# Performance work log

Measured on AMD Instinct MI355X. Metric: run time of the kernel, lower is better.

The kernel has to match this reference:

```python
import jax, jax.numpy as jnp
import numpy as np

HIDDEN = 1024
FFN = 3584
N_EXPERTS = 8
TOP_K = 2


def setup_inputs() -> dict:
    key = jax.random.key(0)
    ks = jax.random.split(key, 5)
    B, S = 2, 2048
    hidden_states = jax.random.normal(ks[0], (B, S, HIDDEN), dtype=jnp.float32)
    # gate: Linear(hidden, n_experts, bias=False); stored as [H, E] so y = x @ gate_w
    gate_w = jax.random.normal(ks[1], (HIDDEN, N_EXPERTS), dtype=jnp.float32) * (HIDDEN ** -0.5)
    # stacked expert weights: w1 (gate proj), w3 (up proj): [E, H, F]; w2 (down proj): [E, F, H]
    w1 = jax.random.normal(ks[2], (N_EXPERTS, HIDDEN, FFN), dtype=jnp.float32) * (HIDDEN ** -0.5)
    w3 = jax.random.normal(ks[3], (N_EXPERTS, HIDDEN, FFN), dtype=jnp.float32) * (HIDDEN ** -0.5)
    w2 = jax.random.normal(ks[4], (N_EXPERTS, FFN, HIDDEN), dtype=jnp.float32) * (FFN ** -0.5)
    return {"hidden_states": hidden_states, "gate_w": gate_w, "w1": w1, "w2": w2, "w3": w3}


def reference(hidden_states, gate_w, w1, w2, w3):
    B, S, H = hidden_states.shape
    x = hidden_states.reshape(-1, H)  # [T, H]
    T = x.shape[0]
    router_logits = x @ gate_w  # [T, E]
    # softmax in fp32 as in original
    routing_weights = jax.nn.softmax(router_logits.astype(jnp.float32), axis=-1)
    top_w, selected = jax.lax.top_k(routing_weights, TOP_K)  # [T, k]
    top_w = top_w / jnp.sum(top_w, axis=-1, keepdims=True)
    top_w = top_w.astype(x.dtype)
    # scatter top-k weights into dense per-expert combine weights [T, E];
    # zero weight for unselected experts reproduces the sparse gather/scatter math exactly
    combine = jnp.zeros((T, N_EXPERTS), dtype=x.dtype).at[
        jnp.arange(T)[:, None], selected
    ].add(top_w)
    # expert gated MLP, all experts batched: [T, E, F]
    g = jnp.einsum('th,ehf->tef', x, w1)
    u = jnp.einsum('th,ehf->tef', x, w3)
    h = jax.nn.silu(g) * u
    # down-proj fused with weighted combine: avoids [T, E, H] intermediate
    final_hidden_states = jnp.einsum('tef,efh,te->th', h, w2, combine)
    return final_hidden_states, router_logits
```

## Files before the change

kernel.cpp:

```cpp
#include <hip/hip_runtime.h>
#include <hip/hip_bf16.h>
#include <cstdint>
#include <cstddef>

#define T_TOK 4096
#define HID   1024
#define FFN   3584
#define FFI   (2 * FFN)
#define NEXP  8
#define RTOT  (T_TOK * 2)
#define MAXT  72
#define BM 128
#define BN 128
#define BK 64
#define NT1 (FFI / BN)
#define NT2 (HID / BN)
#define SPLITK2 2
#define KCH2 (FFN / SPLITK2)
#define CPAD 32
#define G1BLKS (NT1 * MAXT)
#define W2TBLKS ((HID/64)*(FFN/64)*NEXP)
#define RTRBLKS (T_TOK / 4)
#define DTBLKS  ((FFN/64)*(HID/64)*2*NEXP)

typedef __attribute__((ext_vector_type(8))) short bvec8;
typedef __attribute__((ext_vector_type(4))) short bvec4;
typedef __attribute__((ext_vector_type(4))) float fvec4;
typedef unsigned short u16;

__device__ __forceinline__ u16 f2b(float f) {
  __bf16 b = (__bf16)f;
  return __builtin_bit_cast(u16, b);
}
__device__ __forceinline__ float b2f(u16 u) {
  unsigned v = (unsigned)u << 16;
  return __builtin_bit_cast(float, v);
}

__device__ __forceinline__ void gload16(const u16* g, u16* l) {
  __builtin_amdgcn_global_load_lds((const __attribute__((address_space(1))) void*)g,
                                   (__attribute__((address_space(3))) void*)l, 16, 0, 0);
}

__device__ __forceinline__ int xcd_swz(int bid, int nwg) {
  int q = nwg >> 3, r = nwg & 7;
  int xcd = bid & 7, sub = bid >> 3;
  return (xcd < r ? xcd * (q + 1) : r * (q + 1) + (xcd - r) * q) + sub;
}


__device__ void router_body(const float* __restrict__ x, const float* __restrict__ gw,
                            float* __restrict__ logits, int* __restrict__ tk_id,
                            float* __restrict__ tk_w, int* __restrict__ counts,
                            u16* __restrict__ xb, int blk, int tid) {
  const int lane = tid & 63;
  const int wid  = tid >> 6;
  const int t = blk * 4 + wid;
  const float4* xr = (const float4*)(x + (size_t)t * HID);
  float acc[NEXP] = {0.f, 0.f, 0.f, 0.f, 0.f, 0.f, 0.f, 0.f};
#pragma unroll
  for (int it = 0; it < 4; ++it) {
    int k4 = it * 64 + lane;
    float4 xv = xr[k4];
    if (xb) {
      bvec4 o;
      o[0] = (short)f2b(xv.x); o[1] = (short)f2b(xv.y);
      o[2] = (short)f2b(xv.z); o[3] = (short)f2b(xv.w);
      *(bvec4*)(xb + (size_t)t * HID + k4 * 4) = o;
    }
    const float* gp = gw + (size_t)k4 * 4 * NEXP;
    float xs[4] = {xv.x, xv.y, xv.z, xv.w};
#pragma unroll
    for (int kk = 0; kk < 4; ++kk) {
      float4 ga = ((const float4*)(gp + kk * NEXP))[0];
      float4 gb = ((const float4*)(gp + kk * NEXP))[1];
      acc[0] += xs[kk] * ga.x; acc[1] += xs[kk] * ga.y;
      acc[2] += xs[kk] * ga.z; acc[3] += xs[kk] * ga.w;
      acc[4] += xs[kk] * gb.x; acc[5] += xs[kk] * gb.y;
      acc[6] += xs[kk] * gb.z; acc[7] += xs[kk] * gb.w;
    }
  }
#pragma unroll
  for (int off = 32; off > 0; off >>= 1) {
#pragma unroll
    for (int e = 0; e < NEXP; ++e) acc[e] += __shfl_xor(acc[e], off, 64);
  }
  if (lane < NEXP) logits[(size_t)t * NEXP + lane] = acc[lane];
  if (tk_id && lane == 0) {
    int e0 = 0; float l0 = acc[0];
#pragma unroll
    for (int e = 1; e < NEXP; ++e) if (acc[e] > l0) { l0 = acc[e]; e0 = e; }
    int e1 = -1; float l1 = -3.4e38f;
#pragma unroll
    for (int e = 0; e < NEXP; ++e) if (e != e0 && acc[e] > l1) { l1 = acc[e]; e1 = e; }
    float w0 = 1.f / (1.f + expf(l1 - l0));
    float w1 = 1.f - w0;
    tk_id[t * 2 + 0] = e0; tk_id[t * 2 + 1] = e1;
    tk_w[t * 2 + 0] = w0;  tk_w[t * 2 + 1] = w1;
    atomicAdd(&counts[e0 * CPAD], 1); atomicAdd(&counts[e1 * CPAD], 1);
  }
}

__device__ void dualT_body(const float* __restrict__ w1, const float* __restrict__ w3,
                           u16* __restrict__ bi, int bx, int by, int bz, int t,
                           u16* __restrict__ tile) {
  const int e = bz >> 1, half = bz & 1;
  const float* src = (half ? w3 : w1) + (size_t)e * HID * FFN;
  u16* dst = bi + (size_t)e * FFI * HID;
  const int c0 = bx * 64, r0 = by * 64;
  const int m = t & 15;
  const int g = t >> 4;
  u16 v[4][4];
#pragma unroll
  for (int i = 0; i < 4; ++i) {
    float4 q = *(const float4*)(src + (size_t)(r0 + 4 * g + i) * FFN + c0 + 4 * m);
    v[i][0] = f2b(q.x); v[i][1] = f2b(q.y); v[i][2] = f2b(q.z); v[i][3] = f2b(q.w);
  }
  const int phys = (g ^ ((m & 3) << 2)) * 4;
#pragma unroll
  for (int j = 0; j < 4; ++j) {
    int c = 4 * m + j;
    bvec4 o; o[0] = (short)v[0][j]; o[1] = (short)v[1][j];
    o[2] = (short)v[2][j]; o[3] = (short)v[3][j];
    *(bvec4*)&tile[c * 72 + phys] = o;
  }
  __syncthreads();
  const int cl = t >> 2;
  const int q  = t & 3;
  const int base = ((q ^ ((cl >> 2) & 3)) << 4);
  bvec8 ra = *(const bvec8*)&tile[cl * 72 + base];
  bvec8 rb = *(const bvec8*)&tile[cl * 72 + base + 8];
  const int orow = (c0 << 1) + ((cl >> 4) << 5) + (cl & 15) + (half << 4);
  u16* dp = dst + (size_t)orow * HID + r0 + 16 * q;
  *(bvec8*)(dp + 0) = ra;
  *(bvec8*)(dp + 8) = rb;
}

__device__ void w2T_body(const float* __restrict__ w2, u16* __restrict__ w2t,
                         int bx, int by, int e, int t, u16* __restrict__ tile) {
  const float* src = w2 + (size_t)e * FFN * HID;
  u16* dst = w2t + (size_t)e * HID * FFN;
  const int c0 = bx * 64, r0 = by * 64;
  const int m = t & 15;
  const int g = t >> 4;
  u16 v[4][4];
#pragma unroll
  for (int i = 0; i < 4; ++i) {
    float4 q = *(const float4*)(src + (size_t)(r0 + 4 * g + i) * HID + c0 + 4 * m);
    v[i][0] = f2b(q.x); v[i][1] = f2b(q.y); v[i][2] = f2b(q.z); v[i][3] = f2b(q.w);
  }
  const int phys = (g ^ ((m & 3) << 2)) * 4;
#pragma unroll
  for (int j = 0; j < 4; ++j) {
    int c = 4 * m + j;
    bvec4 o; o[0] = (short)v[0][j]; o[1] = (short)v[1][j];
    o[2] = (short)v[2][j]; o[3] = (short)v[3][j];
    *(bvec4*)&tile[c * 72 + phys] = o;
  }
  __syncthreads();
  const int cl = t >> 2;
  const int q  = t & 3;
  const int base = ((q ^ ((cl >> 2) & 3)) << 4);
  bvec8 ra = *(const bvec8*)&tile[cl * 72 + base];
  bvec8 rb = *(const bvec8*)&tile[cl * 72 + base + 8];
  u16* dp = dst + (size_t)(c0 + cl) * FFN + r0 + 16 * q;
  *(bvec8*)(dp + 0) = ra;
  *(bvec8*)(dp + 8) = rb;
}

__device__ void gemm1_body(const u16* __restrict__ xb, const u16* __restrict__ bi,
                           const int* __restrict__ rowmap, const int4* __restrict__ tilemap,
                           u16* __restrict__ hbuf, int bid, int tid,
                           u16* __restrict__ As, u16* __restrict__ Bs) {
  const int wg = xcd_swz(bid, NT1 * MAXT);
  const int mt = wg % MAXT;
  const int nt = wg / MAXT;
  int4 ti = tilemap[mt];
  if (ti.x < 0) return;
  const int e = ti.x, rowbase = ti.y, mvalid = ti.z;
  const int n0 = nt * BN;

  const int lane = tid & 63;
  const int wv = tid >> 6;
  const int srow = tid >> 3;
  const int csrc = ((tid & 7) ^ (srow & 7)) * 8;
  const u16* wb = bi + (size_t)e * FFI * HID;
  const u16* gA[4]; const u16* gB[4];
  u16* lA[4]; u16* lB[4];
#pragma unroll
  for (int r = 0; r < 4; ++r) {
    int row = r * 32 + srow;
    int tok = rowmap[min(rowbase + row, RTOT - 1)];
    gA[r] = xb + (size_t)tok * HID + csrc;
    gB[r] = wb + (size_t)(n0 + row) * HID + csrc;
    lA[r] = &As[(r * 32 + wv * 8) * BK];
    lB[r] = &Bs[(r * 32 + wv * 8) * BK];
  }

  const int wm = (tid >> 7) & 1, wn = (tid >> 6) & 1;
  const int l15 = lane & 15;
  const int kg = lane >> 4;
  const int swz = l15 & 7;
  const int aBase = (wm * 64 + l15) * BK;
  const int bBase = (wn * 64 + l15) * BK;
  const int ch0 = ((0 + kg) ^ swz) * 8;
  const int ch1 = ((4 + kg) ^ swz) * 8;

  fvec4 acc[4][4] = {};

  for (int kt = 0; kt < HID / BK; ++kt) {
#pragma unroll
    for (int r = 0; r < 4; ++r) { gload16(gA[r], lA[r]); gA[r] += BK; }
#pragma unroll
    for (int r = 0; r < 4; ++r) { gload16(gB[r], lB[r]); gB[r] += BK; }
    __syncthreads();
    bvec8 a0[4], a1[4];
#pragma unroll
    for (int mi = 0; mi < 4; ++mi) {
      a0[mi] = *(const bvec8*)&As[aBase + mi * 16 * BK + ch0];
      a1[mi] = *(const bvec8*)&As[aBase + mi * 16 * BK + ch1];
    }
#pragma unroll
    for (int ni = 0; ni < 4; ++ni) {
      bvec8 b0 = *(const bvec8*)&Bs[bBase + ni * 16 * BK + ch0];
#pragma unroll
      for (int mi = 0; mi < 4; ++mi)
        acc[mi][ni] = __builtin_amdgcn_mfma_f32_16x16x32_bf16(a0[mi], b0, acc[mi][ni], 0, 0, 0);
      bvec8 b1 = *(const bvec8*)&Bs[bBase + ni * 16 * BK + ch1];
#pragma unroll
      for (int mi = 0; mi < 4; ++mi)
        acc[mi][ni] = __builtin_amdgcn_mfma_f32_16x16x32_bf16(a1[mi], b1, acc[mi][ni], 0, 0, 0);
    }
    __syncthreads();
  }
  const int rg4 = (lane >> 4) * 4;
#pragma unroll
  for (int mi = 0; mi < 4; ++mi) {
#pragma unroll
    for (int j = 0; j < 4; ++j) {
      int ml = wm * 64 + mi * 16 + rg4 + j;
      if (ml < mvalid) {
        size_t rowoff = (size_t)(rowbase + ml) * FFN + ((n0 + wn * 64) >> 1);
#pragma unroll
        for (int np = 0; np < 2; ++np) {
          float g = acc[mi][2 * np][j], u = acc[mi][2 * np + 1][j];
          float hv = (g / (1.f + expf(-g))) * u;
          hbuf[rowoff + np * 16 + l15] = f2b(hv);
        }
      }
    }
  }
}


__global__ void fused_pre_kernel(const float* __restrict__ x, const float* __restrict__ gw,
                                 const float* __restrict__ w1, const float* __restrict__ w3,
                                 float* __restrict__ logits, int* __restrict__ tk_id,
                                 float* __restrict__ tk_w, int* __restrict__ counts,
                                 u16* __restrict__ xb, u16* __restrict__ bi) {
  __shared__ __attribute__((aligned(16))) u16 tile[64 * 72];
  const int bid = blockIdx.x;
  if (bid < RTRBLKS) {
    router_body(x, gw, logits, tk_id, tk_w, counts, xb, bid, threadIdx.x);
  } else {
    int did = bid - RTRBLKS;
    int bx = did % (FFN / 64); int rest = did / (FFN / 64);
    int by = rest % (HID / 64); int bz = rest / (HID / 64);
    dualT_body(w1, w3, bi, bx, by, bz, threadIdx.x, tile);
  }
}

__launch_bounds__(256, 3)
__global__ void fused_g1w2_kernel(const u16* __restrict__ xb, const u16* __restrict__ bi,
                                  const int* __restrict__ rowmap,
                                  const int4* __restrict__ tilemap, u16* __restrict__ hbuf,
                                  const float* __restrict__ w2, u16* __restrict__ w2t) {
  __shared__ __attribute__((aligned(128))) u16 As[BM * BK];
  __shared__ __attribute__((aligned(128))) u16 Bs[BN * BK];
  const int bid = blockIdx.x;
  if (bid < G1BLKS) {
    gemm1_body(xb, bi, rowmap, tilemap, hbuf, bid, threadIdx.x, As, Bs);
  } else {
    int id = bid - G1BLKS;
    int bx = id % (HID / 64); int rest = id / (HID / 64);
    int by = rest % (FFN / 64); int e = rest / (FFN / 64);
    w2T_body(w2, w2t, bx, by, e, threadIdx.x, As);
  }
}

__global__ void router_kernel(const float* __restrict__ x, const float* __restrict__ gw,
                              float* __restrict__ logits, int* __restrict__ tk_id,
                              float* __restrict__ tk_w, int* __restrict__ counts,
                              u16* __restrict__ xb) {
  router_body(x, gw, logits, tk_id, tk_w, counts, xb, blockIdx.x, threadIdx.x);
}
__global__ void transpose_cast_dual_kernel(const float* __restrict__ w1,
                                           const float* __restrict__ w3,
                                           u16* __restrict__ bi) {
  __shared__ __attribute__((aligned(16))) u16 tile[64 * 72];
  dualT_body(w1, w3, bi, blockIdx.x, blockIdx.y, blockIdx.z, threadIdx.x, tile);
}
__global__ void transpose_cast_w2_kernel(const float* __restrict__ w2, u16* __restrict__ w2t) {
  __shared__ __attribute__((aligned(16))) u16 tile[64 * 72];
  w2T_body(w2, w2t, blockIdx.x, blockIdx.y, blockIdx.z, threadIdx.x, tile);
}
__launch_bounds__(256, 3)
__global__ void gemm1_kernel(const u16* __restrict__ xb, const u16* __restrict__ bi,
                             const int* __restrict__ rowmap,
                             const int4* __restrict__ tilemap, u16* __restrict__ hbuf) {
  __shared__ __attribute__((aligned(128))) u16 As[BM * BK];
  __shared__ __attribute__((aligned(128))) u16 Bs[BN * BK];
  gemm1_body(xb, bi, rowmap, tilemap, hbuf, blockIdx.x, threadIdx.x, As, Bs);
}

__global__ void scan_kernel(const int* __restrict__ counts, int* __restrict__ offsets,
                            int* __restrict__ cursors, int4* __restrict__ tilemap) {
  __shared__ int c[NEXP];
  __shared__ int tbase[NEXP + 1];
  const int t = threadIdx.x;
  if (t < NEXP) c[t] = counts[t * CPAD];
  __syncthreads();
  if (t < NEXP) {
    int off = 0, tiles = 0;
    for (int e = 0; e < t; ++e) { off += c[e]; tiles += (c[e] + BM - 1) / BM; }
    offsets[t] = off; cursors[t * CPAD] = 0;
    if (t == NEXP - 1) {
      offsets[NEXP] = off + c[t];
      tbase[NEXP] = tiles + (c[t] + BM - 1) / BM;
    }
    tbase[t] = tiles;
    const int cc = c[t];
    for (int tm = 0; tm * BM < cc; ++tm)
      tilemap[tiles + tm] = make_int4(t, off + tm * BM, min(BM, cc - tm * BM), 0);
  }
  __syncthreads();
  for (int i = tbase[NEXP] + t; i < MAXT; i += 64)
    tilemap[i] = make_int4(-1, 0, 0, 0);
}

__global__ void scatter_kernel(const int* __restrict__ tk_id, const float* __restrict__ tk_w,
                               const int* __restrict__ offsets, int* __restrict__ cursors,
                               int* __restrict__ rowmap, float* __restrict__ roww,
                               int* __restrict__ tokrow) {
  int i = blockIdx.x * 256 + threadIdx.x;
  int t = i >> 1;
  int e = tk_id[i]; float w = tk_w[i];
  const int lane = threadIdx.x & 63;
  const unsigned long long lt = (lane == 63) ? ~0ull >> 1 : (1ull << lane) - 1ull;
  int base = 0, rank = 0;
#pragma unroll
  for (int ex = 0; ex < NEXP; ++ex) {
    unsigned long long m = __ballot(e == ex);
    if (e == ex) {
      int cnt = __popcll(m);
      int leader = __ffsll((long long)m) - 1;
      int b = 0;
      if (lane == leader) b = atomicAdd(&cursors[ex * CPAD], cnt);
      b = __shfl(b, leader, 64);
      base = b; rank = __popcll(m & lt);
    }
  }
  int r = offsets[e] + base + rank;
  rowmap[r] = t; roww[r] = w;
  tokrow[i] = r;
}

__launch_bounds__(256, 3)
__global__ void gemm2_kernel(const u16* __restrict__ hbuf, const u16* __restrict__ w2t,
                             const float* __restrict__ roww,
                             const int4* __restrict__ tilemap, u16* __restrict__ part) {
  const int wg = xcd_swz(blockIdx.x, NT2 * MAXT * SPLITK2);
  const int mt = wg % MAXT;
  const int rest = wg / MAXT;
  const int nt = rest % NT2;
  const int sk = rest / NT2;
  int4 ti = tilemap[mt];
  if (ti.x < 0) return;
  const int e = ti.x, rowbase = ti.y, mvalid = ti.z;
  const int n0 = nt * BN;
  const int k0 = sk * KCH2;

  __shared__ __attribute__((aligned(128))) u16 As[BM * BK];
  __shared__ __attribute__((aligned(128))) u16 Bs[BN * BK];

  const int tid = threadIdx.x;
  const int lane = tid & 63;
  const int wv = tid >> 6;

  const int srow = tid >> 3;
  const int csrc = ((tid & 7) ^ (srow & 7)) * 8;
  const u16* wb2 = w2t + (size_t)e * HID * FFN;
  const u16* gA[4]; const u16* gB[4];
  u16* lA[4]; u16* lB[4];
#pragma unroll
  for (int r = 0; r < 4; ++r) {
    int row = r * 32 + srow;
    gA[r] = hbuf + (size_t)min(rowbase + row, RTOT - 1) * FFN + k0 + csrc;
    gB[r] = wb2 + (size_t)(n0 + row) * FFN + k0 + csrc;
    lA[r] = &As[(r * 32 + wv * 8) * BK];
    lB[r] = &Bs[(r * 32 + wv * 8) * BK];
  }

  const int wm = (tid >> 7) & 1, wn = (tid >> 6) & 1;
  const int l15 = lane & 15;
  const int kg = lane >> 4;
  const int swz = l15 & 7;
  const int aBase = (wm * 64 + l15) * BK;
  const int bBase = (wn * 64 + l15) * BK;
  const int ch0 = ((0 + kg) ^ swz) * 8;
  const int ch1 = ((4 + kg) ^ swz) * 8;

  fvec4 acc[4][4] = {};

  for (int kt = 0; kt < KCH2 / BK; ++kt) {
#pragma unroll
    for (int r = 0; r < 4; ++r) { gload16(gA[r], lA[r]); gA[r] += BK; }
#pragma unroll
    for (int r = 0; r < 4; ++r) { gload16(gB[r], lB[r]); gB[r] += BK; }
    __syncthreads();
    bvec8 a0[4], a1[4];
#pragma unroll
    for (int mi = 0; mi < 4; ++mi) {
      a0[mi] = *(const bvec8*)&As[aBase + mi * 16 * BK + ch0];
      a1[mi] = *(const bvec8*)&As[aBase + mi * 16 * BK + ch1];
    }
#pragma unroll
    for (int ni = 0; ni < 4; ++ni) {
      bvec8 b0 = *(const bvec8*)&Bs[bBase + ni * 16 * BK + ch0];
#pragma unroll
      for (int mi = 0; mi < 4; ++mi)
        acc[mi][ni] = __builtin_amdgcn_mfma_f32_16x16x32_bf16(a0[mi], b0, acc[mi][ni], 0, 0, 0);
      bvec8 b1 = *(const bvec8*)&Bs[bBase + ni * 16 * BK + ch1];
#pragma unroll
      for (int mi = 0; mi < 4; ++mi)
        acc[mi][ni] = __builtin_amdgcn_mfma_f32_16x16x32_bf16(a1[mi], b1, acc[mi][ni], 0, 0, 0);
    }
    __syncthreads();
  }
  u16* pp = part + (size_t)sk * RTOT * HID;
  const int rg4 = (lane >> 4) * 4;
#pragma unroll
  for (int mi = 0; mi < 4; ++mi) {
#pragma unroll
    for (int j = 0; j < 4; ++j) {
      int ml = wm * 64 + mi * 16 + rg4 + j;
      if (ml < mvalid) {
        int r = rowbase + ml;
        float wgt = roww[r];
        u16* op = pp + (size_t)r * HID + n0 + wn * 64;
#pragma unroll
        for (int ni = 0; ni < 4; ++ni)
          op[ni * 16 + l15] = f2b(acc[mi][ni][j] * wgt);
      }
    }
  }
}

__global__ void combine_kernel(const u16* __restrict__ part, const int* __restrict__ tokrow,
                               float* __restrict__ out) {
  int idx = blockIdx.x * 256 + threadIdx.x;
  int t = idx >> 7;
  int c = (idx & 127) * 8;
  int r0 = tokrow[2 * t], r1 = tokrow[2 * t + 1];
  const size_t sk1 = (size_t)RTOT * HID;
  bvec8 a = *(const bvec8*)(part + (size_t)r0 * HID + c);
  bvec8 b = *(const bvec8*)(part + sk1 + (size_t)r0 * HID + c);
  bvec8 d = *(const bvec8*)(part + (size_t)r1 * HID + c);
  bvec8 f = *(const bvec8*)(part + sk1 + (size_t)r1 * HID + c);
  float* dst = out + (size_t)t * HID + c;
#pragma unroll
  for (int k = 0; k < 8; ++k)
    dst[k] = (b2f((u16)a[k]) + b2f((u16)b[k])) + (b2f((u16)d[k]) + b2f((u16)f[k]));
}

extern "C" void kernel_launch(void* const* d_in, const int* in_sizes, int n_in,
                              void* d_out, int out_size, void* d_ws, size_t ws_size,
                              hipStream_t stream) {
  (void)in_sizes; (void)n_in; (void)out_size;
  const float* x  = (const float*)d_in[0];
  const float* gw = (const float*)d_in[1];
  const float* w1 = (const float*)d_in[2];
  const float* w2 = (const float*)d_in[3];
  const float* w3 = (const float*)d_in[4];
  float* out = (float*)d_out;
  float* logits = out + (size_t)T_TOK * HID;

  size_t off = 0;
  auto take = [&](size_t b) { size_t o = off; off += (b + 255) & ~(size_t)255; return o; };
  size_t o_xb   = take((size_t)T_TOK * HID * 2);
  size_t o_wt   = take((size_t)NEXP * FFI * HID * 2);
  size_t o_hb   = take((size_t)RTOT * FFN * 2);
  size_t o_rmap = take((size_t)RTOT * 4);
  size_t o_rw   = take((size_t)RTOT * 4);
  size_t o_tid  = take((size_t)RTOT * 4);
  size_t o_tw   = take((size_t)RTOT * 4);
  size_t o_trow = take((size_t)RTOT * 4);
  size_t o_cnt  = take(4 * NEXP * CPAD);
  size_t o_ofs  = take(4 * (NEXP + 1));
  size_t o_cur  = take(4 * NEXP * CPAD);
  size_t o_tmap = take(MAXT * 16);
  size_t total_base = off;
  size_t o_w2t  = take((size_t)NEXP * HID * FFN * 2);
  size_t total_fused = off;

  if (ws_size < total_base) {
    hipMemsetAsync(d_out, 0, (size_t)T_TOK * HID * sizeof(float), stream);
    router_kernel<<<RTRBLKS, 256, 0, stream>>>(x, gw, logits, nullptr, nullptr, nullptr,
                                               nullptr);
    return;
  }
  const bool fused = (ws_size >= total_fused);

  char* w = (char*)d_ws;
  u16* xb   = (u16*)(w + o_xb);
  u16* bi   = (u16*)(w + o_wt);
  u16* part = bi + (size_t)NEXP * HID * FFN;
  u16* hb   = (u16*)(w + o_hb);
  int*   rmap = (int*)(w + o_rmap);
  float* rw   = (float*)(w + o_rw);
  int*   tkid = (int*)(w + o_tid);
  float* tkw  = (float*)(w + o_tw);
  int*   trow = (int*)(w + o_trow);
  int*   cnt  = (int*)(w + o_cnt);
  int*   ofs  = (int*)(w + o_ofs);
  int*   cur  = (int*)(w + o_cur);
  int4*  tmap = (int4*)(w + o_tmap);
  u16* w2t = fused ? (u16*)(w + o_w2t) : bi;

  hipMemsetAsync(cnt, 0, 4 * NEXP * CPAD, stream);
  if (fused) {
    fused_pre_kernel<<<RTRBLKS + DTBLKS, 256, 0, stream>>>(x, gw, w1, w3, logits, tkid, tkw,
                                                           cnt, xb, bi);
    scan_kernel<<<1, 64, 0, stream>>>(cnt, ofs, cur, tmap);
    scatter_kernel<<<RTOT / 256, 256, 0, stream>>>(tkid, tkw, ofs, cur, rmap, rw, trow);
    fused_g1w2_kernel<<<G1BLKS + W2TBLKS, 256, 0, stream>>>(xb, bi, rmap, tmap, hb, w2, w2t);
  } else {
    router_kernel<<<RTRBLKS, 256, 0, stream>>>(x, gw, logits, tkid, tkw, cnt, xb);
    scan_kernel<<<1, 64, 0, stream>>>(cnt, ofs, cur, tmap);
    scatter_kernel<<<RTOT / 256, 256, 0, stream>>>(tkid, tkw, ofs, cur, rmap, rw, trow);
    transpose_cast_dual_kernel<<<dim3(FFN / 64, HID / 64, 2 * NEXP), 256, 0, stream>>>(w1, w3, bi);
    gemm1_kernel<<<G1BLKS, 256, 0, stream>>>(xb, bi, rmap, tmap, hb);
    transpose_cast_w2_kernel<<<dim3(HID / 64, FFN / 64, NEXP), 256, 0, stream>>>(w2, w2t);
  }
  gemm2_kernel<<<NT2 * MAXT * SPLITK2, 256, 0, stream>>>(hb, w2t, rw, tmap, part);
  combine_kernel<<<T_TOK * HID / 8 / 256, 256, 0, stream>>>(part, trow, out);
}
```

Baseline: 385.0 us.

## Double-buffer LDS tiles in expert GEMMs to overlap loads with MFMA

Both expert GEMMs now keep two LDS buffers for the A and B tiles. The next k-tile is prefetched with global_load_lds while MFMAs run on the current one, and the two __syncthreads per iteration become a single vmcnt wait plus barrier. Wave priority is raised around the MFMA block. This doubles LDS use to 64KB per block, which can lower occupancy below the launch_bounds target of 3 blocks.

Measured after the change: 493.1 us. 1.28x slower.

```diff
diff --git a/kernel.cpp b/kernel.cpp
--- a/kernel.cpp
+++ b/kernel.cpp
@@ -22,6 +22,8 @@
 #define W2TBLKS ((HID/64)*(FFN/64)*NEXP)
 #define RTRBLKS (T_TOK / 4)
 #define DTBLKS  ((FFN/64)*(HID/64)*2*NEXP)
+#define ATILE (BM * BK)
+#define BTILE (BN * BK)
 
 typedef __attribute__((ext_vector_type(8))) short bvec8;
 typedef __attribute__((ext_vector_type(4))) short bvec4;
@@ -171,7 +173,7 @@
 __device__ void gemm1_body(const u16* __restrict__ xb, const u16* __restrict__ bi,
                            const int* __restrict__ rowmap, const int4* __restrict__ tilemap,
                            u16* __restrict__ hbuf, int bid, int tid,
-                           u16* __restrict__ As, u16* __restrict__ Bs) {
+                           u16* __restrict__ AsBase, u16* __restrict__ BsBase) {
   const int wg = xcd_swz(bid, NT1 * MAXT);
   const int mt = wg % MAXT;
   const int nt = wg / MAXT;
@@ -186,16 +188,24 @@
   const int csrc = ((tid & 7) ^ (srow & 7)) * 8;
   const u16* wb = bi + (size_t)e * FFI * HID;
   const u16* gA[4]; const u16* gB[4];
-  u16* lA[4]; u16* lB[4];
+  int lofs[4];
 #pragma unroll
   for (int r = 0; r < 4; ++r) {
     int row = r * 32 + srow;
     int tok = rowmap[min(rowbase + row, RTOT - 1)];
     gA[r] = xb + (size_t)tok * HID + csrc;
     gB[r] = wb + (size_t)(n0 + row) * HID + csrc;
-    lA[r] = &As[(r * 32 + wv * 8) * BK];
-    lB[r] = &Bs[(r * 32 + wv * 8) * BK];
-  }
+    lofs[r] = (r * 32 + wv * 8) * BK;
+  }
+
+  auto STAGE = [&](int t) {
+    u16* Ab = AsBase + (t & 1) * ATILE;
+    u16* Bb = BsBase + (t & 1) * BTILE;
+#pragma unroll
+    for (int r = 0; r < 4; ++r) gload16(gA[r] + t * BK, &Ab[lofs[r]]);
+#pragma unroll
+    for (int r = 0; r < 4; ++r) gload16(gB[r] + t * BK, &Bb[lofs[r]]);
+  };
 
   const int wm = (tid >> 7) & 1, wn = (tid >> 6) & 1;
   const int l15 = lane & 15;
@@ -208,18 +218,21 @@
 
   fvec4 acc[4][4] = {};
 
+  STAGE(0);
+  asm volatile("s_waitcnt vmcnt(0)" ::: "memory");
+  __builtin_amdgcn_s_barrier();
+
   for (int kt = 0; kt < HID / BK; ++kt) {
-#pragma unroll
-    for (int r = 0; r < 4; ++r) { gload16(gA[r], lA[r]); gA[r] += BK; }
-#pragma unroll
-    for (int r = 0; r < 4; ++r) { gload16(gB[r], lB[r]); gB[r] += BK; }
-    __syncthreads();
+    const u16* As = AsBase + (kt & 1) * ATILE;
+    const u16* Bs = BsBase + (kt & 1) * BTILE;
+    if (kt + 1 < HID / BK) STAGE(kt + 1);
     bvec8 a0[4], a1[4];
 #pragma unroll
     for (int mi = 0; mi < 4; ++mi) {
       a0[mi] = *(const bvec8*)&As[aBase + mi * 16 * BK + ch0];
       a1[mi] = *(const bvec8*)&As[aBase + mi * 16 * BK + ch1];
     }
+    __builtin_amdgcn_s_setprio(1);
 #pragma unroll
     for (int ni = 0; ni < 4; ++ni) {
       bvec8 b0 = *(const bvec8*)&Bs[bBase + ni * 16 * BK + ch0];
@@ -231,7 +244,9 @@
       for (int mi = 0; mi < 4; ++mi)
         acc[mi][ni] = __builtin_amdgcn_mfma_f32_16x16x32_bf16(a1[mi], b1, acc[mi][ni], 0, 0, 0);
     }
-    __syncthreads();
+    __builtin_amdgcn_s_setprio(0);
+    asm volatile("s_waitcnt vmcnt(0)" ::: "memory");
+    __builtin_amdgcn_s_barrier();
   }
   const int rg4 = (lane >> 4) * 4;
 #pragma unroll
@@ -275,16 +290,16 @@
                                   const int* __restrict__ rowmap,
                                   const int4* __restrict__ tilemap, u16* __restrict__ hbuf,
                                   const float* __restrict__ w2, u16* __restrict__ w2t) {
-  __shared__ __attribute__((aligned(128))) u16 As[BM * BK];
-  __shared__ __attribute__((aligned(128))) u16 Bs[BN * BK];
+  __shared__ __attribute__((aligned(128))) u16 As[2][ATILE];
+  __shared__ __attribute__((aligned(128))) u16 Bs[2][BTILE];
   const int bid = blockIdx.x;
   if (bid < G1BLKS) {
-    gemm1_body(xb, bi, rowmap, tilemap, hbuf, bid, threadIdx.x, As, Bs);
+    gemm1_body(xb, bi, rowmap, tilemap, hbuf, bid, threadIdx.x, As[0], Bs[0]);
   } else {
     int id = bid - G1BLKS;
     int bx = id % (HID / 64); int rest = id / (HID / 64);
     int by = rest % (FFN / 64); int e = rest / (FFN / 64);
-    w2T_body(w2, w2t, bx, by, e, threadIdx.x, As);
+    w2T_body(w2, w2t, bx, by, e, threadIdx.x, As[0]);
   }
 }
 
@@ -308,9 +323,9 @@
 __global__ void gemm1_kernel(const u16* __restrict__ xb, const u16* __restrict__ bi,
                              const int* __restrict__ rowmap,
                              const int4* __restrict__ tilemap, u16* __restrict__ hbuf) {
-  __shared__ __attribute__((aligned(128))) u16 As[BM * BK];
-  __shared__ __attribute__((aligned(128))) u16 Bs[BN * BK];
-  gemm1_body(xb, bi, rowmap, tilemap, hbuf, blockIdx.x, threadIdx.x, As, Bs);
+  __shared__ __attribute__((aligned(128))) u16 As[2][ATILE];
+  __shared__ __attribute__((aligned(128))) u16 Bs[2][BTILE];
+  gemm1_body(xb, bi, rowmap, tilemap, hbuf, blockIdx.x, threadIdx.x, As[0], Bs[0]);
 }
 
 __global__ void scan_kernel(const int* __restrict__ counts, int* __restrict__ offsets,
@@ -380,8 +395,8 @@
   const int n0 = nt * BN;
   const int k0 = sk * KCH2;
 
-  __shared__ __attribute__((aligned(128))) u16 As[BM * BK];
-  __shared__ __attribute__((aligned(128))) u16 Bs[BN * BK];
+  __shared__ __attribute__((aligned(128))) u16 As[2][ATILE];
+  __shared__ __attribute__((aligned(128))) u16 Bs[2][BTILE];
 
   const int tid = threadIdx.x;
   const int lane = tid & 63;
@@ -391,15 +406,23 @@
   const int csrc = ((tid & 7) ^ (srow & 7)) * 8;
   const u16* wb2 = w2t + (size_t)e * HID * FFN;
   const u16* gA[4]; const u16* gB[4];
-  u16* lA[4]; u16* lB[4];
+  int lofs[4];
 #pragma unroll
   for (int r = 0; r < 4; ++r) {
     int row = r * 32 + srow;
     gA[r] = hbuf + (size_t)min(rowbase + row, RTOT - 1) * FFN + k0 + csrc;
     gB[r] = wb2 + (size_t)(n0 + row) * FFN + k0 + csrc;
-    lA[r] = &As[(r * 32 + wv * 8) * BK];
-    lB[r] = &Bs[(r * 32 + wv * 8) * BK];
-  }
+    lofs[r] = (r * 32 + wv * 8) * BK;
+  }
+
+  auto STAGE = [&](int t) {
+    u16* Ab = As[t & 1];
+    u16* Bb = Bs[t & 1];
+#pragma unroll
+    for (int r = 0; r < 4; ++r) gload16(gA[r] + t * BK, &Ab[lofs[r]]);
+#pragma unroll
+    for (int r = 0; r < 4; ++r) gload16(gB[r] + t * BK, &Bb[lofs[r]]);
+  };
 
   const int wm = (tid >> 7) & 1, wn = (tid >> 6) & 1;
   const int l15 = lane & 15;
@@ -412,30 +435,35 @@
 
   fvec4 acc[4][4] = {};
 
+  STAGE(0);
+  asm volatile("s_waitcnt vmcnt(0)" ::: "memory");
+  __builtin_amdgcn_s_barrier();
+
   for (int kt = 0; kt < KCH2 / BK; ++kt) {
-#pragma unroll
-    for (int r = 0; r < 4; ++r) { gload16(gA[r], lA[r]); gA[r] += BK; }
-#pragma unroll
-    for (int r = 0; r < 4; ++r) { gload16(gB[r], lB[r]); gB[r] += BK; }
-    __syncthreads();
+    const u16* Ac = As[kt & 1];
+    const u16* Bc = Bs[kt & 1];
+    if (kt + 1 < KCH2 / BK) STAGE(kt + 1);
     bvec8 a0[4], a1[4];
 #pragma unroll
     for (int mi = 0; mi < 4; ++mi) {
-      a0[mi] = *(const bvec8*)&As[aBase + mi * 16 * BK + ch0];
-      a1[mi] = *(const bvec8*)&As[aBase + mi * 16 * BK + ch1];
-    }
+      a0[mi] = *(const bvec8*)&Ac[aBase + mi * 16 * BK + ch0];
+      a1[mi] = *(const bvec8*)&Ac[aBase + mi * 16 * BK + ch1];
+    }
+    __builtin_amdgcn_s_setprio(1);
 #pragma unroll
     for (int ni = 0; ni < 4; ++ni) {
-      bvec8 b0 = *(const bvec8*)&Bs[bBase + ni * 16 * BK + ch0];
+      bvec8 b0 = *(const bvec8*)&Bc[bBase + ni * 16 * BK + ch0];
 #pragma unroll
       for (int mi = 0; mi < 4; ++mi)
         acc[mi][ni] = __builtin_amdgcn_mfma_f32_16x16x32_bf16(a0[mi], b0, acc[mi][ni], 0, 0, 0);
-      bvec8 b1 = *(const bvec8*)&Bs[bBase + ni * 16 * BK + ch1];
+      bvec8 b1 = *(const bvec8*)&Bc[bBase + ni * 16 * BK + ch1];
 #pragma unroll
       for (int mi = 0; mi < 4; ++mi)
         acc[mi][ni] = __builtin_amdgcn_mfma_f32_16x16x32_bf16(a1[mi], b1, acc[mi][ni], 0, 0, 0);
     }
-    __syncthreads();
+    __builtin_amdgcn_s_setprio(0);
+    asm volatile("s_waitcnt vmcnt(0)" ::: "memory");
+    __builtin_amdgcn_s_barrier();
   }
   u16* pp = part + (size_t)sk * RTOT * HID;
   const int rg4 = (lane >> 4) * 4;
```
